# Kernel tuning notes

Hardware: AMD Instinct MI355X
Metric: run time of the kernel (lower is better)

Reference implementation:

```python
import jax, jax.numpy as jnp
import numpy as np

E = 8        # num_local_experts
H = 2048     # hidden_size
I = 4096     # intermediate_size
TOP_K = 1    # num_experts_per_tok
B, S = 2, 1024


def setup_inputs() -> dict:
    key = jax.random.key(0)
    ks = jax.random.split(key, 8)
    sc = 0.02
    return {
        "hidden_states": jax.random.normal(ks[0], (B, S, H), dtype=jnp.float32),
        "router_w": jax.random.normal(ks[1], (E, H), dtype=jnp.float32) * sc,      # torch Linear weight [out,in]
        "gate_up_proj": jax.random.normal(ks[2], (E, H, 2 * I), dtype=jnp.float32) * sc,
        "down_proj": jax.random.normal(ks[3], (E, I, H), dtype=jnp.float32) * sc,
        "shared_gate": jax.random.normal(ks[4], (H, I), dtype=jnp.float32) * sc,
        "shared_up": jax.random.normal(ks[5], (H, I), dtype=jnp.float32) * sc,
        "shared_down": jax.random.normal(ks[6], (I, H), dtype=jnp.float32) * sc,
    }


def reference(hidden_states, router_w, gate_up_proj, down_proj, shared_gate, shared_up, shared_down):
    x = hidden_states.reshape(-1, H)                      # [T, H]
    T = x.shape[0]

    # Router: top-k logits kept, rest -> -inf, then sigmoid (Llama4 sigmoid routing)
    logits = jnp.einsum('th,eh->te', x, router_w)          # [T, E]
    topv, topi = jax.lax.top_k(logits, TOP_K)
    scores = jnp.full_like(logits, -jnp.inf)
    scores = scores.at[jnp.arange(T)[:, None], topi].set(topv)
    router_scores = jax.nn.sigmoid(scores.astype(jnp.float32)).astype(x.dtype).T  # [E, T]

    # Dense dispatch: every token goes to every expert, scaled by its (mostly-zero) score
    routed_in = x[None, :, :] * router_scores[:, :, None]  # [E, T, H]

    # Per-expert gated MLP as one grouped einsum
    gu = jnp.einsum('eth,ehf->etf', routed_in, gate_up_proj)   # [E, T, 2I]
    gate, up = gu[..., :I], gu[..., I:]
    routed_out = jnp.einsum('eti,eih->eth', jax.nn.silu(gate) * up, down_proj)  # [E, T, H]

    # Shared expert on raw tokens
    shared = (jax.nn.silu(x @ shared_gate) * (x @ shared_up)) @ shared_down     # [T, H]

    # scatter_add over full index range == sum over expert axis
    out = shared + routed_out.sum(axis=0)
    return out, router_scores
```

## Files before the change

kernel.cpp:

```cpp
#include <hip/hip_runtime.h>
#include <hip/hip_bf16.h>

#define NE 8
#define TT 2048
#define HD 2048
#define ID 4096

typedef __attribute__((ext_vector_type(8))) short bf16x8;
typedef __attribute__((ext_vector_type(4))) float f32x4;
typedef __attribute__((ext_vector_type(4))) unsigned int u32x4;
typedef __attribute__((ext_vector_type(2))) unsigned int u32x2;
typedef __attribute__((ext_vector_type(4))) unsigned short u16x4;
typedef __attribute__((ext_vector_type(8))) unsigned short u16x8;

__device__ __forceinline__ unsigned short f2bf(float f) {
  return __builtin_bit_cast(unsigned short, __float2bfloat16(f));
}

__global__ void init_kernel(int* counts) {
  if (threadIdx.x < NE) counts[threadIdx.x] = 0;
}

__global__ __launch_bounds__(256) void router_kernel(
    const float* __restrict__ x, const float* __restrict__ rw,
// ... 19 lines not shown
  __shared__ float part[4][NE];
  __shared__ int sE;
  __shared__ float sS;
  const int wave = tid >> 6, lane = tid & 63;
  if (lane == 0) {
#pragma unroll
    for (int e = 0; e < NE; ++e) part[wave][e] = acc[e];
  }
  __syncthreads();
  if (tid == 0) {
    float best = -3.4e38f;
    int be = 0;
#pragma unroll
    for (int e = 0; e < NE; ++e) {
      float v = part[0][e] + part[1][e] + part[2][e] + part[3][e];
      if (v > best) { best = v; be = e; }
    }
    float s = 1.f / (1.f + expf(-best));
    sE = be;
    sS = s;
    int pos = atomicAdd(&counts[be], 1);
    tlist[be * TT + pos] = t;
  }
  __syncthreads();
  if (tid < NE) rs_out[tid * TT + t] = (tid == sE) ? sS : 0.f;
  const float s = sS;
  for (int h = tid; h < HD; h += 256) {
    float f = xr[h];
    xb[(size_t)t * HD + h] = f2bf(f);
    xsb[(size_t)t * HD + h] = f2bf(f * s);
  }
}

__global__ __launch_bounds__(256) void tconv_kernel(
    const float* __restrict__ shg, const float* __restrict__ shu,
    const float* __restrict__ shd, unsigned short* __restrict__ shgT,
    unsigned short* __restrict__ shuT, unsigned short* __restrict__ shdT) {
  const int z = blockIdx.z;
  const float* src;
  unsigned short* dst;
  int K, N;
  if (z == 0)      { src = shg; dst = shgT; K = HD; N = ID; }
  else if (z == 1) { src = shu; dst = shuT; K = HD; N = ID; }
  else             { src = shd; dst = shdT; K = ID; N = HD; }
  const int kb = blockIdx.y * 64, nb = blockIdx.x * 64;
  if (kb >= K || nb >= N) return;
  __shared__ unsigned short tile[64][68];
  const int tid = threadIdx.x;
  const int rr = tid >> 4, cc = (tid & 15) * 4;
#pragma unroll
  for (int it = 0; it < 4; ++it) {
    int r = rr + it * 16;
    f32x4 v = *(const f32x4*)(const void*)(src + (size_t)(kb + r) * N + nb + cc);
    tile[r][cc + 0] = f2bf(v[0]);
    tile[r][cc + 1] = f2bf(v[1]);
    tile[r][cc + 2] = f2bf(v[2]);
    tile[r][cc + 3] = f2bf(v[3]);
  }
  __syncthreads();
  const int nr = tid >> 2, kc = (tid & 3) * 16;
#pragma unroll
  for (int h = 0; h < 2; ++h) {
    u16x8 w;
#pragma unroll
    for (int j = 0; j < 8; ++j) w[j] = tile[kc + h * 8 + j][nr];
    *(u16x8*)(void*)(dst + (size_t)(nb + nr) * K + kb + kc + h * 8) = w;
  }
}

__global__ __launch_bounds__(256) void gu_routed_kernel(
    const unsigned short* __restrict__ xsb, const float* __restrict__ gup,
    const int* __restrict__ counts, const int* __restrict__ tlist,
    unsigned short* __restrict__ hrt) {
  const int e = blockIdx.z;
  const int cnt = counts[e];
  const int row0 = blockIdx.y * 128;
  if (row0 >= cnt) return;
  const int n0 = blockIdx.x * 64;
  const float* Bb = gup + (size_t)e * HD * (2 * ID);
  const float* B1 = Bb + n0;
  const float* B2 = Bb + ID + n0;
  const size_t ldb = 2 * ID;

  __shared__ int toks[128];
  __shared__ __align__(16) unsigned short As[2][128][40];
  __shared__ __align__(16) unsigned short Bg[2][64][36];
  __shared__ __align__(16) unsigned short Bu[2][64][36];

  const int tid = threadIdx.x;
  if (tid < 128) {
    int r = row0 + tid;
    toks[tid] = (r < cnt) ? tlist[e * TT + r] : -1;
  }
  __syncthreads();

  const int lane = tid & 63, wave = tid >> 6;
  const int wm = (wave >> 1) * 64, wn = (wave & 1) * 32;
  const int rA0 = tid >> 2, cA = (tid & 3) * 8, rA1 = rA0 + 64;
  const int tok0 = toks[rA0], tok1 = toks[rA1];
  const unsigned short* ap0 = xsb + ((tok0 >= 0) ? (size_t)tok0 * HD : 0) + cA;
  const unsigned short* ap1 = xsb + ((tok1 >= 0) ? (size_t)tok1 * HD : 0) + cA;
  const int nB = tid & 63;
  const int kq0 = tid >> 6;
// ... 73 lines not shown
#pragma unroll
      for (int nt = 0; nt < 2; ++nt) {
        accg[mt][nt] = __builtin_amdgcn_mfma_f32_16x16x32_bf16(af[mt], bgf[nt], accg[mt][nt], 0, 0, 0);
        accu[mt][nt] = __builtin_amdgcn_mfma_f32_16x16x32_bf16(af[mt], bud[nt], accu[mt][nt], 0, 0, 0);
      }
    __builtin_amdgcn_s_setprio(0);
    __builtin_amdgcn_sched_barrier(0);
    if (t + 1 < NT) WR(cur ^ 1);
    if (t + 2 < NT) LD((t + 2) * 32);
    asm volatile("s_waitcnt lgkmcnt(0)" ::: "memory");
    __builtin_amdgcn_sched_barrier(0);
    __builtin_amdgcn_s_barrier();
  }
#undef LD
#undef WR

#pragma unroll
  for (int mt = 0; mt < 4; ++mt)
#pragma unroll
    for (int nt = 0; nt < 2; ++nt)
#pragma unroll
      for (int r = 0; r < 4; ++r) {
        int ml = wm + mt * 16 + q * 4 + r;
        if (row0 + ml < cnt) {
          int tok = toks[ml];
          int n = n0 + wn + nt * 16 + fm;
          float g = accg[mt][nt][r], u = accu[mt][nt][r];
          float hv = g / (1.f + __expf(-g)) * u;
          hrt[(size_t)tok * ID + n] = f2bf(hv);
        }
      }
}

template <int BF>
__global__ __launch_bounds__(256) void gu_shared_kernel(
    const unsigned short* __restrict__ xb, const float* __restrict__ shg,
    const float* __restrict__ shu, const unsigned short* __restrict__ shgT,
    const unsigned short* __restrict__ shuT, unsigned short* __restrict__ hsh) {
  const int row0 = blockIdx.y * 128;
  const int n0 = blockIdx.x * 64;
  const float* B1 = shg + n0;
  const float* B2 = shu + n0;
  const size_t ldb = ID;
  const unsigned short* T1 = shgT + (size_t)n0 * HD;
  const unsigned short* T2 = shuT + (size_t)n0 * HD;

  __shared__ __align__(16) unsigned short As[2][128][40];
  __shared__ __align__(16) unsigned short Bg[2][64][36];
  __shared__ __align__(16) unsigned short Bu[2][64][36];

  const int tid = threadIdx.x;
  const int lane = tid & 63, wave = tid >> 6;
  const int wm = (wave >> 1) * 64, wn = (wave & 1) * 32;
  const int rA0 = tid >> 2, cA = (tid & 3) * 8, rA1 = rA0 + 64;
  const unsigned short* ap0 = xb + (size_t)(row0 + rA0) * HD + cA;
  const unsigned short* ap1 = xb + (size_t)(row0 + rA1) * HD + cA;
  const int nB = tid & 63;
  const int kq0 = tid >> 6;
  const int fm = lane & 15, q = lane >> 4;
  const int nrT = tid >> 2, kcT = (tid & 3) * 8;

  const f32x4 zf = {0.f, 0.f, 0.f, 0.f};
  f32x4 accg[4][2], accu[4][2];
#pragma unroll
  for (int a = 0; a < 4; ++a)
#pragma unroll
    for (int b = 0; b < 2; ++b) { accg[a][b] = zf; accu[a][b] = zf; }

  u32x4 ra0, ra1, tb1, tb2;
  f32x4 rg0, rg1, ru0, ru1;

#define LD(K0)                                                                 \
  do {                                                                         \
    ra0 = *(const u32x4*)(const void*)(ap0 + (K0));                            \
    ra1 = *(const u32x4*)(const void*)(ap1 + (K0));                            \
    if constexpr (BF) {                                                        \
      tb1 = *(const u32x4*)(const void*)(T1 + (size_t)nrT * HD + (K0) + kcT);  \
      tb2 = *(const u32x4*)(const void*)(T2 + (size_t)nrT * HD + (K0) + kcT);  \
    } else {                                                                   \
      const float* p1 = B1 + (size_t)((K0) + kq0 * 4) * ldb + nB;              \
      const float* p1b = p1 + 16 * ldb;                                        \
      rg0[0] = p1[0]; rg0[1] = p1[ldb]; rg0[2] = p1[2 * ldb]; rg0[3] = p1[3 * ldb]; \
      rg1[0] = p1b[0]; rg1[1] = p1b[ldb]; rg1[2] = p1b[2 * ldb]; rg1[3] = p1b[3 * ldb]; \
      const float* p2 = B2 + (size_t)((K0) + kq0 * 4) * ldb + nB;              \
      const float* p2b = p2 + 16 * ldb;                                        \
      ru0[0] = p2[0]; ru0[1] = p2[ldb]; ru0[2] = p2[2 * ldb]; ru0[3] = p2[3 * ldb]; \
      ru1[0] = p2b[0]; ru1[1] = p2b[ldb]; ru1[2] = p2b[2 * ldb]; ru1[3] = p2b[3 * ldb]; \
    }                                                                          \
  } while (0)

#define WR(BUF)                                                                \
  do {                                                                         \
    *(u32x4*)(void*)&As[BUF][rA0][cA] = ra0;                                   \
    *(u32x4*)(void*)&As[BUF][rA1][cA] = ra1;                                   \
    if constexpr (BF) {                                                        \
      u32x2 lo, hi;                                                            \
      lo[0] = tb1[0]; lo[1] = tb1[1]; hi[0] = tb1[2]; hi[1] = tb1[3];          \
      *(u32x2*)(void*)&Bg[BUF][nrT][kcT] = lo;                                 \
      *(u32x2*)(void*)&Bg[BUF][nrT][kcT + 4] = hi;                             \
      lo[0] = tb2[0]; lo[1] = tb2[1]; hi[0] = tb2[2]; hi[1] = tb2[3];          \
      *(u32x2*)(void*)&Bu[BUF][nrT][kcT] = lo;                                 \
      *(u32x2*)(void*)&Bu[BUF][nrT][kcT + 4] = hi;                             \
    } else {                                                                   \
      u16x4 w;                                                                 \
      w[0] = f2bf(rg0[0]); w[1] = f2bf(rg0[1]); w[2] = f2bf(rg0[2]); w[3] = f2bf(rg0[3]); \
      *(u16x4*)(void*)&Bg[BUF][nB][kq0 * 4] = w;                               \
      w[0] = f2bf(rg1[0]); w[1] = f2bf(rg1[1]); w[2] = f2bf(rg1[2]); w[3] = f2bf(rg1[3]); \
      *(u16x4*)(void*)&Bg[BUF][nB][kq0 * 4 + 16] = w;                          \
      w[0] = f2bf(ru0[0]); w[1] = f2bf(ru0[1]); w[2] = f2bf(ru0[2]); w[3] = f2bf(ru0[3]); \
      *(u16x4*)(void*)&Bu[BUF][nB][kq0 * 4] = w;                               \
      w[0] = f2bf(ru1[0]); w[1] = f2bf(ru1[1]); w[2] = f2bf(ru1[2]); w[3] = f2bf(ru1[3]); \
      *(u16x4*)(void*)&Bu[BUF][nB][kq0 * 4 + 16] = w;                          \
    }                                                                          \
  } while (0)

  LD(0);
  WR(0);
  LD(32);
  asm volatile("s_waitcnt lgkmcnt(0)" ::: "memory");
  __builtin_amdgcn_sched_barrier(0);
  __builtin_amdgcn_s_barrier();

  constexpr int NT = HD / 32;
  for (int t = 0; t < NT; ++t) {
    const int cur = t & 1;
    bf16x8 af[4], bgf[2], bud[2];
#pragma unroll
    for (int mt = 0; mt < 4; ++mt)
      af[mt] = __builtin_bit_cast(bf16x8,
               *(const u32x4*)(const void*)&As[cur][wm + mt * 16 + fm][q * 8]);
#pragma unroll
    for (int nt = 0; nt < 2; ++nt) {
      const unsigned short* bp = &Bg[cur][wn + nt * 16 + fm][q * 8];
      u32x2 lo = *(const u32x2*)(const void*)bp;
      u32x2 hi = *(const u32x2*)(const void*)(bp + 4);
      u32x4 v; v[0] = lo[0]; v[1] = lo[1]; v[2] = hi[0]; v[3] = hi[1];
      bgf[nt] = __builtin_bit_cast(bf16x8, v);
      const unsigned short* bp2 = &Bu[cur][wn + nt * 16 + fm][q * 8];
      lo = *(const u32x2*)(const void*)bp2;
      hi = *(const u32x2*)(const void*)(bp2 + 4);
      v[0] = lo[0]; v[1] = lo[1]; v[2] = hi[0]; v[3] = hi[1];
      bud[nt] = __builtin_bit_cast(bf16x8, v);
    }
    __builtin_amdgcn_s_setprio(1);
#pragma unroll
    for (int mt = 0; mt < 4; ++mt)
#pragma unroll
      for (int nt = 0; nt < 2; ++nt) {
        accg[mt][nt] = __builtin_amdgcn_mfma_f32_16x16x32_bf16(af[mt], bgf[nt], accg[mt][nt], 0, 0, 0);
        accu[mt][nt] = __builtin_amdgcn_mfma_f32_16x16x32_bf16(af[mt], bud[nt], accu[mt][nt], 0, 0, 0);
      }
    __builtin_amdgcn_s_setprio(0);
    __builtin_amdgcn_sched_barrier(0);
    if (t + 1 < NT) WR(cur ^ 1);
    if (t + 2 < NT) LD((t + 2) * 32);
    asm volatile("s_waitcnt lgkmcnt(0)" ::: "memory");
    __builtin_amdgcn_sched_barrier(0);
    __builtin_amdgcn_s_barrier();
  }
#undef LD
#undef WR

#pragma unroll
  for (int mt = 0; mt < 4; ++mt)
#pragma unroll
    for (int nt = 0; nt < 2; ++nt)
#pragma unroll
      for (int r = 0; r < 4; ++r) {
        int row = row0 + wm + mt * 16 + q * 4 + r;
        int n = n0 + wn + nt * 16 + fm;
        float g = accg[mt][nt][r], u = accu[mt][nt][r];
        float hv = g / (1.f + __expf(-g)) * u;
        hsh[(size_t)row * ID + n] = f2bf(hv);
      }
}

template <int BF>
__global__ __launch_bounds__(256) void dn_shared_kernel(
    const unsigned short* __restrict__ hsh, const float* __restrict__ shd,
    const unsigned short* __restrict__ shdT, float* __restrict__ out) {
  const int row0 = blockIdx.y * 128;
  const int n0 = blockIdx.x * 64;
  const float* B = shd + n0;
  const unsigned short* T = shdT + (size_t)n0 * ID;

  __shared__ __align__(16) unsigned short As[2][128][40];
  __shared__ __align__(16) unsigned short Bs[2][64][36];

  const int tid = threadIdx.x;
  const int lane = tid & 63, wave = tid >> 6;
  const int wm = (wave >> 1) * 64, wn = (wave & 1) * 32;
  const int rA0 = tid >> 2, cA = (tid & 3) * 8, rA1 = rA0 + 64;
  const unsigned short* ap0 = hsh + (size_t)(row0 + rA0) * ID + cA;
  const unsigned short* ap1 = hsh + (size_t)(row0 + rA1) * ID + cA;
  const int nB = tid & 63;
  const int kq0 = tid >> 6;
  const int fm = lane & 15, q = lane >> 4;
  const int nrT = tid >> 2, kcT = (tid & 3) * 8;

  const f32x4 zf = {0.f, 0.f, 0.f, 0.f};
  f32x4 acc[4][2];
#pragma unroll
  for (int a = 0; a < 4; ++a)
#pragma unroll
    for (int b = 0; b < 2; ++b) acc[a][b] = zf;

  u32x4 ra0, ra1, tb;
  f32x4 rb0, rb1;

#define LD(K0)                                                                 \
  do {                                                                         \
    ra0 = *(const u32x4*)(const void*)(ap0 + (K0));                            \
    ra1 = *(const u32x4*)(const void*)(ap1 + (K0));                            \
    if constexpr (BF) {                                                        \
      tb = *(const u32x4*)(const void*)(T + (size_t)nrT * ID + (K0) + kcT);    \
    } else {                                                                   \
      const float* p = B + (size_t)((K0) + kq0 * 4) * HD + nB;                 \
      const float* pb = p + 16 * HD;                                           \
      rb0[0] = p[0]; rb0[1] = p[HD]; rb0[2] = p[2 * HD]; rb0[3] = p[3 * HD];   \
      rb1[0] = pb[0]; rb1[1] = pb[HD]; rb1[2] = pb[2 * HD]; rb1[3] = pb[3 * HD]; \
    }                                                                          \
  } while (0)

#define WR(BUF)                                                                \
  do {                                                                         \
    *(u32x4*)(void*)&As[BUF][rA0][cA] = ra0;                                   \
    *(u32x4*)(void*)&As[BUF][rA1][cA] = ra1;                                   \
    if constexpr (BF) {                                                        \
      u32x2 lo, hi;                                                            \
      lo[0] = tb[0]; lo[1] = tb[1]; hi[0] = tb[2]; hi[1] = tb[3];              \
      *(u32x2*)(void*)&Bs[BUF][nrT][kcT] = lo;                                 \
      *(u32x2*)(void*)&Bs[BUF][nrT][kcT + 4] = hi;                             \
    } else {                                                                   \
      u16x4 w;                                                                 \
      w[0] = f2bf(rb0[0]); w[1] = f2bf(rb0[1]); w[2] = f2bf(rb0[2]); w[3] = f2bf(rb0[3]); \
      *(u16x4*)(void*)&Bs[BUF][nB][kq0 * 4] = w;                               \
      w[0] = f2bf(rb1[0]); w[1] = f2bf(rb1[1]); w[2] = f2bf(rb1[2]); w[3] = f2bf(rb1[3]); \
      *(u16x4*)(void*)&Bs[BUF][nB][kq0 * 4 + 16] = w;                          \
    }                                                                          \
  } while (0)

  LD(0);
  WR(0);
  LD(32);
  asm volatile("s_waitcnt lgkmcnt(0)" ::: "memory");
  __builtin_amdgcn_sched_barrier(0);
  __builtin_amdgcn_s_barrier();

  constexpr int NT = ID / 32;
  for (int t = 0; t < NT; ++t) {
    const int cur = t & 1;
    bf16x8 af[4], bfr[2];
#pragma unroll
    for (int mt = 0; mt < 4; ++mt)
      af[mt] = __builtin_bit_cast(bf16x8,
               *(const u32x4*)(const void*)&As[cur][wm + mt * 16 + fm][q * 8]);
#pragma unroll
    for (int nt = 0; nt < 2; ++nt) {
      const unsigned short* bp = &Bs[cur][wn + nt * 16 + fm][q * 8];
      u32x2 lo = *(const u32x2*)(const void*)bp;
      u32x2 hi = *(const u32x2*)(const void*)(bp + 4);
      u32x4 v; v[0] = lo[0]; v[1] = lo[1]; v[2] = hi[0]; v[3] = hi[1];
      bfr[nt] = __builtin_bit_cast(bf16x8, v);
    }
    __builtin_amdgcn_s_setprio(1);
#pragma unroll
    for (int mt = 0; mt < 4; ++mt)
#pragma unroll
      for (int nt = 0; nt < 2; ++nt)
        acc[mt][nt] = __builtin_amdgcn_mfma_f32_16x16x32_bf16(af[mt], bfr[nt], acc[mt][nt], 0, 0, 0);
    __builtin_amdgcn_s_setprio(0);
    __builtin_amdgcn_sched_barrier(0);
    if (t + 1 < NT) WR(cur ^ 1);
    if (t + 2 < NT) LD((t + 2) * 32);
    asm volatile("s_waitcnt lgkmcnt(0)" ::: "memory");
    __builtin_amdgcn_sched_barrier(0);
    __builtin_amdgcn_s_barrier();
  }
#undef LD
#undef WR

#pragma unroll
  for (int mt = 0; mt < 4; ++mt)
#pragma unroll
    for (int nt = 0; nt < 2; ++nt)
#pragma unroll
      for (int r = 0; r < 4; ++r) {
        int row = row0 + wm + mt * 16 + q * 4 + r;
        int n = n0 + wn + nt * 16 + fm;
        out[(size_t)row * HD + n] = acc[mt][nt][r];
      }
}

__global__ __launch_bounds__(256) void dn_routed_kernel(
    const unsigned short* __restrict__ hrt, const float* __restrict__ dwn,
    const int* __restrict__ counts, const int* __restrict__ tlist,
    float* __restrict__ out) {
  const int e = blockIdx.z;
  const int cnt = counts[e];
  const int row0 = blockIdx.y * 128;
  if (row0 >= cnt) return;
  const int n0 = blockIdx.x * 64;
  const float* B = dwn + (size_t)e * ID * HD + n0;

  __shared__ int toks[128];
  __shared__ __align__(16) unsigned short As[2][128][40];
  __shared__ __align__(16) unsigned short Bs[2][64][36];

  const int tid = threadIdx.x;
  if (tid < 128) {
    int r = row0 + tid;
    toks[tid] = (r < cnt) ? tlist[e * TT + r] : -1;
  }
  __syncthreads();

  const int lane = tid & 63, wave = tid >> 6;
  const int wm = (wave >> 1) * 64, wn = (wave & 1) * 32;
  const int rA0 = tid >> 2, cA = (tid & 3) * 8, rA1 = rA0 + 64;
  const int tok0 = toks[rA0], tok1 = toks[rA1];
  const unsigned short* ap0 = hrt + ((tok0 >= 0) ? (size_t)tok0 * ID : 0) + cA;
  const unsigned short* ap1 = hrt + ((tok1 >= 0) ? (size_t)tok1 * ID : 0) + cA;
  const int nB = tid & 63;
  const int kq0 = tid >> 6;
  const int fm = lane & 15, q = lane >> 4;

  const f32x4 zf = {0.f, 0.f, 0.f, 0.f};
  const u32x4 z4 = {0u, 0u, 0u, 0u};
  f32x4 acc[4][2];
#pragma unroll
  for (int a = 0; a < 4; ++a)
#pragma unroll
    for (int b = 0; b < 2; ++b) acc[a][b] = zf;

  u32x4 ra0, ra1;
  f32x4 rb0, rb1;

#define LD(K0)                                                                 \
  do {                                                                         \
    ra0 = (tok0 >= 0) ? *(const u32x4*)(const void*)(ap0 + (K0)) : z4;         \
    ra1 = (tok1 >= 0) ? *(const u32x4*)(const void*)(ap1 + (K0)) : z4;         \
    const float* p = B + (size_t)((K0) + kq0 * 4) * HD + nB;                   \
    const float* pb = p + 16 * HD;                                             \
    rb0[0] = p[0]; rb0[1] = p[HD]; rb0[2] = p[2 * HD]; rb0[3] = p[3 * HD];     \
    rb1[0] = pb[0]; rb1[1] = pb[HD]; rb1[2] = pb[2 * HD]; rb1[3] = pb[3 * HD]; \
  } while (0)

#define WR(BUF)                                                                \
  do {                                                                         \
    *(u32x4*)(void*)&As[BUF][rA0][cA] = ra0;                                   \
    *(u32x4*)(void*)&As[BUF][rA1][cA] = ra1;                                   \
    u16x4 w;                                                                   \
    w[0] = f2bf(rb0[0]); w[1] = f2bf(rb0[1]); w[2] = f2bf(rb0[2]); w[3] = f2bf(rb0[3]); \
    *(u16x4*)(void*)&Bs[BUF][nB][kq0 * 4] = w;                                 \
    w[0] = f2bf(rb1[0]); w[1] = f2bf(rb1[1]); w[2] = f2bf(rb1[2]); w[3] = f2bf(rb1[3]); \
    *(u16x4*)(void*)&Bs[BUF][nB][kq0 * 4 + 16] = w;                            \
  } while (0)

  LD(0);
  WR(0);
  LD(32);
  asm volatile("s_waitcnt lgkmcnt(0)" ::: "memory");
  __builtin_amdgcn_sched_barrier(0);
  __builtin_amdgcn_s_barrier();

  constexpr int NT = ID / 32;
  for (int t = 0; t < NT; ++t) {
    const int cur = t & 1;
    bf16x8 af[4], bfr[2];
#pragma unroll
    for (int mt = 0; mt < 4; ++mt)
      af[mt] = __builtin_bit_cast(bf16x8,
               *(const u32x4*)(const void*)&As[cur][wm + mt * 16 + fm][q * 8]);
#pragma unroll
    for (int nt = 0; nt < 2; ++nt) {
      const unsigned short* bp = &Bs[cur][wn + nt * 16 + fm][q * 8];
      u32x2 lo = *(const u32x2*)(const void*)bp;
      u32x2 hi = *(const u32x2*)(const void*)(bp + 4);
      u32x4 v; v[0] = lo[0]; v[1] = lo[1]; v[2] = hi[0]; v[3] = hi[1];
      bfr[nt] = __builtin_bit_cast(bf16x8, v);
    }
    __builtin_amdgcn_s_setprio(1);
#pragma unroll
    for (int mt = 0; mt < 4; ++mt)
#pragma unroll
      for (int nt = 0; nt < 2; ++nt)
        acc[mt][nt] = __builtin_amdgcn_mfma_f32_16x16x32_bf16(af[mt], bfr[nt], acc[mt][nt], 0, 0, 0);
    __builtin_amdgcn_s_setprio(0);
    __builtin_amdgcn_sched_barrier(0);
    if (t + 1 < NT) WR(cur ^ 1);
    if (t + 2 < NT) LD((t + 2) * 32);
    asm volatile("s_waitcnt lgkmcnt(0)" ::: "memory");
    __builtin_amdgcn_sched_barrier(0);
    __builtin_amdgcn_s_barrier();
  }
#undef LD
#undef WR

#pragma unroll
  for (int mt = 0; mt < 4; ++mt)
#pragma unroll
    for (int nt = 0; nt < 2; ++nt)
#pragma unroll
      for (int r = 0; r < 4; ++r) {
        int ml = wm + mt * 16 + q * 4 + r;
        if (row0 + ml < cnt) {
          int tok = toks[ml];
          int n = n0 + wn + nt * 16 + fm;
          out[(size_t)tok * HD + n] += acc[mt][nt][r];
        }
      }
}

extern "C" void kernel_launch(void* const* d_in, const int* in_sizes, int n_in,
                              void* d_out, int out_size, void* d_ws, size_t ws_size,
                              hipStream_t stream) {
  const float* x   = (const float*)d_in[0];
  const float* rw  = (const float*)d_in[1];
  const float* gup = (const float*)d_in[2];
  const float* dwn = (const float*)d_in[3];
  const float* shg = (const float*)d_in[4];
  const float* shu = (const float*)d_in[5];
  const float* shd = (const float*)d_in[6];
  float* out = (float*)d_out;

  char* ws = (char*)d_ws;
  int* counts = (int*)ws;
  int* tlist = (int*)(ws + 1024);
  unsigned short* xb  = (unsigned short*)(ws + (1 << 17));
  unsigned short* xsb = (unsigned short*)(ws + (1 << 17) + 8388608);
  unsigned short* hsh = (unsigned short*)(ws + (1 << 17) + 16777216);
  unsigned short* hrt = (unsigned short*)(ws + (1 << 17) + 33554432);
  const size_t WB = (size_t)(1 << 17) + 50331648;
  unsigned short* shgT = (unsigned short*)(ws + WB);
  unsigned short* shuT = (unsigned short*)(ws + WB + 16777216);
  unsigned short* shdT = (unsigned short*)(ws + WB + 33554432);
  const size_t need = WB + 3ull * 16777216ull;
  const int shbf = (ws_size >= need) ? 1 : 0;

  hipLaunchKernelGGL(init_kernel, dim3(1), dim3(64), 0, stream, counts);
  hipLaunchKernelGGL(router_kernel, dim3(TT), dim3(256), 0, stream,
                     x, rw, out + (size_t)TT * HD, xb, xsb, counts, tlist);
  if (shbf)
    hipLaunchKernelGGL(tconv_kernel, dim3(64, 64, 3), dim3(256), 0, stream,
                       shg, shu, shd, shgT, shuT, shdT);
  hipLaunchKernelGGL(gu_routed_kernel, dim3(ID / 64, TT / 128, NE), dim3(256), 0, stream,
                     xsb, gup, counts, tlist, hrt);
  if (shbf)
    hipLaunchKernelGGL((gu_shared_kernel<1>), dim3(ID / 64, TT / 128), dim3(256), 0, stream,
                       xb, shg, shu, shgT, shuT, hsh);
  else
    hipLaunchKernelGGL((gu_shared_kernel<0>), dim3(ID / 64, TT / 128), dim3(256), 0, stream,
                       xb, shg, shu, shgT, shuT, hsh);
  if (shbf)
    hipLaunchKernelGGL((dn_shared_kernel<1>), dim3(HD / 64, TT / 128), dim3(256), 0, stream,
                       hsh, shd, shdT, out);
  else
    hipLaunchKernelGGL((dn_shared_kernel<0>), dim3(HD / 64, TT / 128), dim3(256), 0, stream,
                       hsh, shd, shdT, out);
  hipLaunchKernelGGL(dn_routed_kernel, dim3(HD / 64, TT / 128, NE), dim3(256), 0, stream,
                     hrt, dwn, counts, tlist, out);
}
```

Before: 1.313 ms.

## Pre-convert all expert weights to transposed bf16 and merge shared/routed GEMMs

```diff
diff --git a/kernel.cpp b/kernel.cpp
--- a/kernel.cpp
+++ b/kernel.cpp
@@ -75,19 +75,13 @@
   }
 }
 
-__global__ __launch_bounds__(256) void tconv_kernel(
-    const float* __restrict__ shg, const float* __restrict__ shu,
-    const float* __restrict__ shd, unsigned short* __restrict__ shgT,
-    unsigned short* __restrict__ shuT, unsigned short* __restrict__ shdT) {
-  const int z = blockIdx.z;
-  const float* src;
-  unsigned short* dst;
-  int K, N;
-  if (z == 0)      { src = shg; dst = shgT; K = HD; N = ID; }
-  else if (z == 1) { src = shu; dst = shuT; K = HD; N = ID; }
-  else             { src = shd; dst = shdT; K = ID; N = HD; }
+__global__ __launch_bounds__(256) void wconv_kernel(
+    const float* __restrict__ src, unsigned short* __restrict__ dst,
+    const int K, const int N) {
+  const int b = blockIdx.z;
+  src += (size_t)b * K * N;
+  dst += (size_t)b * N * K;
   const int kb = blockIdx.y * 64, nb = blockIdx.x * 64;
-  if (kb >= K || nb >= N) return;
   __shared__ unsigned short tile[64][68];
   const int tid = threadIdx.x;
   const int rr = tid >> 4, cc = (tid & 15) * 4;
@@ -111,7 +105,250 @@
   }
 }
 
-__global__ __launch_bounds__(256) void gu_routed_kernel(
+__global__ __launch_bounds__(256) void gu_kernel(
+    const unsigned short* __restrict__ xb, const unsigned short* __restrict__ xsb,
+    const unsigned short* __restrict__ gupT, const unsigned short* __restrict__ shgT,
+    const unsigned short* __restrict__ shuT, const int* __restrict__ counts,
+    const int* __restrict__ tlist, unsigned short* __restrict__ hsh,
+    unsigned short* __restrict__ hrt) {
+  const int bz = blockIdx.z;
+  const bool sh = (bz == NE);
+  const int cnt = sh ? TT : counts[bz];
+  const int row0 = blockIdx.y * 128;
+  if (row0 >= cnt) return;
+  const int n0 = blockIdx.x * 64;
+  const unsigned short* Aptr = sh ? xb : xsb;
+  const unsigned short* Bg0;
+  const unsigned short* Bu0;
+  if (sh) {
+    Bg0 = shgT + (size_t)n0 * HD;
+    Bu0 = shuT + (size_t)n0 * HD;
+  } else {
+    const unsigned short* base = gupT + (size_t)bz * (2 * ID) * HD;
+    Bg0 = base + (size_t)n0 * HD;
+    Bu0 = base + (size_t)(ID + n0) * HD;
+  }
+  unsigned short* hout = sh ? hsh : hrt;
+
+  __shared__ int toks[128];
+  __shared__ __align__(16) unsigned short As[2][128][40];
+  __shared__ __align__(16) unsigned short Bg[2][64][40];
+  __shared__ __align__(16) unsigned short Bu[2][64][40];
+
+  const int tid = threadIdx.x;
+  if (tid < 128) {
+    int r = row0 + tid;
+    toks[tid] = (r < cnt) ? (sh ? r : tlist[bz * TT + r]) : -1;
+  }
+  __syncthreads();
+
+  const int lane = tid & 63, wave = tid >> 6;
+  const int wm = (wave >> 1) * 64, wn = (wave & 1) * 32;
+  const int rA0 = tid >> 2, cA = (tid & 3) * 8, rA1 = rA0 + 64;
+  const int tok0 = toks[rA0], tok1 = toks[rA1];
+  const unsigned short* ap0 = Aptr + ((tok0 >= 0) ? (size_t)tok0 * HD : 0) + cA;
+  const unsigned short* ap1 = Aptr + ((tok1 >= 0) ? (size_t)tok1 * HD : 0) + cA;
+  const int rB = tid >> 2, cB = (tid & 3) * 8;
+  const unsigned short* pg = Bg0 + (size_t)rB * HD + cB;
+  const unsigned short* pu = Bu0 + (size_t)rB * HD + cB;
+  const int fm = lane & 15, q = lane >> 4;
+
+  const f32x4 zf = {0.f, 0.f, 0.f, 0.f};
+  const u32x4 z4 = {0u, 0u, 0u, 0u};
+  f32x4 accg[4][2], accu[4][2];
+#pragma unroll
+  for (int a = 0; a < 4; ++a)
+#pragma unroll
+    for (int b = 0; b < 2; ++b) { accg[a][b] = zf; accu[a][b] = zf; }
+
+  u32x4 ra0, ra1, rb1, rb2;
+
+#define LD(K0)                                                                 \
+  do {                                                                         \
+    ra0 = (tok0 >= 0) ? *(const u32x4*)(const void*)(ap0 + (K0)) : z4;         \
+    ra1 = (tok1 >= 0) ? *(const u32x4*)(const void*)(ap1 + (K0)) : z4;         \
+    rb1 = *(const u32x4*)(const void*)(pg + (K0));                             \
+    rb2 = *(const u32x4*)(const void*)(pu + (K0));                             \
+  } while (0)
+
+#define WR(BUF)                                                                \
+  do {                                                                         \
+    *(u32x4*)(void*)&As[BUF][rA0][cA] = ra0;                                   \
+    *(u32x4*)(void*)&As[BUF][rA1][cA] = ra1;                                   \
+    *(u32x4*)(void*)&Bg[BUF][rB][cB] = rb1;                                    \
+    *(u32x4*)(void*)&Bu[BUF][rB][cB] = rb2;                                    \
+  } while (0)
+
+  LD(0);
+  WR(0);
+  LD(32);
+  asm volatile("s_waitcnt lgkmcnt(0)" ::: "memory");
+  __builtin_amdgcn_sched_barrier(0);
+  __builtin_amdgcn_s_barrier();
+
+  constexpr int NT = HD / 32;
+  for (int t = 0; t < NT; ++t) {
+    const int cur = t & 1;
+    bf16x8 af[4], bgf[2], bud[2];
+#pragma unroll
+    for (int mt = 0; mt < 4; ++mt)
+      af[mt] = __builtin_bit_cast(bf16x8,
+               *(const u32x4*)(const void*)&As[cur][wm + mt * 16 + fm][q * 8]);
+#pragma unroll
+    for (int nt = 0; nt < 2; ++nt) {
+      bgf[nt] = __builtin_bit_cast(bf16x8,
+                *(const u32x4*)(const void*)&Bg[cur][wn + nt * 16 + fm][q * 8]);
+      bud[nt] = __builtin_bit_cast(bf16x8,
+                *(const u32x4*)(const void*)&Bu[cur][wn + nt * 16 + fm][q * 8]);
+    }
+    __builtin_amdgcn_s_setprio(1);
+#pragma unroll
+    for (int mt = 0; mt < 4; ++mt)
+#pragma unroll
+      for (int nt = 0; nt < 2; ++nt) {
+        accg[mt][nt] = __builtin_amdgcn_mfma_f32_16x16x32_bf16(af[mt], bgf[nt], accg[mt][nt], 0, 0, 0);
+        accu[mt][nt] = __builtin_amdgcn_mfma_f32_16x16x32_bf16(af[mt], bud[nt], accu[mt][nt], 0, 0, 0);
+      }
+    __builtin_amdgcn_s_setprio(0);
+    __builtin_amdgcn_sched_barrier(0);
+    if (t + 1 < NT) WR(cur ^ 1);
+    if (t + 2 < NT) LD((t + 2) * 32);
+    asm volatile("s_waitcnt lgkmcnt(0)" ::: "memory");
+    __builtin_amdgcn_sched_barrier(0);
+    __builtin_amdgcn_s_barrier();
+  }
+#undef LD
+#undef WR
+
+#pragma unroll
+  for (int mt = 0; mt < 4; ++mt)
+#pragma unroll
+    for (int nt = 0; nt < 2; ++nt)
+#pragma unroll
+      for (int r = 0; r < 4; ++r) {
+        int ml = wm + mt * 16 + q * 4 + r;
+        if (row0 + ml < cnt) {
+          int tok = toks[ml];
+          int n = n0 + wn + nt * 16 + fm;
+          float g = accg[mt][nt][r], u = accu[mt][nt][r];
+          float hv = g / (1.f + __expf(-g)) * u;
+          hout[(size_t)tok * ID + n] = f2bf(hv);
+        }
+      }
+}
+
+template <int ROUTED>
+__global__ __launch_bounds__(256) void dn_kernel(
+    const unsigned short* __restrict__ Ah, const unsigned short* __restrict__ BT,
+    const int* __restrict__ counts, const int* __restrict__ tlist,
+    float* __restrict__ out) {
+  const int e = blockIdx.z;
+  const int cnt = ROUTED ? counts[e] : TT;
+  const int row0 = blockIdx.y * 128;
+  if (row0 >= cnt) return;
+  const int n0 = blockIdx.x * 64;
+  const unsigned short* B0 = ROUTED ? (BT + (size_t)e * HD * ID + (size_t)n0 * ID)
+                                    : (BT + (size_t)n0 * ID);
+
+  __shared__ int toks[128];
+  __shared__ __align__(16) unsigned short As[2][128][40];
+  __shared__ __align__(16) unsigned short Bs[2][64][40];
+
+  const int tid = threadIdx.x;
+  if (tid < 128) {
+    int r = row0 + tid;
+    toks[tid] = (r < cnt) ? (ROUTED ? tlist[e * TT + r] : r) : -1;
+  }
+  __syncthreads();
+
+  const int lane = tid & 63, wave = tid >> 6;
+  const int wm = (wave >> 1) * 64, wn = (wave & 1) * 32;
+  const int rA0 = tid >> 2, cA = (tid & 3) * 8, rA1 = rA0 + 64;
+  const int tok0 = toks[rA0], tok1 = toks[rA1];
+  const unsigned short* ap0 = Ah + ((tok0 >= 0) ? (size_t)tok0 * ID : 0) + cA;
+  const unsigned short* ap1 = Ah + ((tok1 >= 0) ? (size_t)tok1 * ID : 0) + cA;
+  const int rB = tid >> 2, cB = (tid & 3) * 8;
+  const unsigned short* pb = B0 + (size_t)rB * ID + cB;
+  const int fm = lane & 15, q = lane >> 4;
+
+  const f32x4 zf = {0.f, 0.f, 0.f, 0.f};
+  const u32x4 z4 = {0u, 0u, 0u, 0u};
+  f32x4 acc[4][2];
+#pragma unroll
+  for (int a = 0; a < 4; ++a)
+#pragma unroll
+    for (int b = 0; b < 2; ++b) acc[a][b] = zf;
+
+  u32x4 ra0, ra1, rb1;
+
+#define LD(K0)                                                                 \
+  do {                                                                         \
+    ra0 = (tok0 >= 0) ? *(const u32x4*)(const void*)(ap0 + (K0)) : z4;         \
+    ra1 = (tok1 >= 0) ? *(const u32x4*)(const void*)(ap1 + (K0)) : z4;         \
+    rb1 = *(const u32x4*)(const void*)(pb + (K0));                             \
+  } while (0)
+
+#define WR(BUF)                                                                \
+  do {                                                                         \
+    *(u32x4*)(void*)&As[BUF][rA0][cA] = ra0;                                   \
+    *(u32x4*)(void*)&As[BUF][rA1][cA] = ra1;                                   \
+    *(u32x4*)(void*)&Bs[BUF][rB][cB] = rb1;                                    \
+  } while (0)
+
+  LD(0);
+  WR(0);
+  LD(32);
+  asm volatile("s_waitcnt lgkmcnt(0)" ::: "memory");
+  __builtin_amdgcn_sched_barrier(0);
+  __builtin_amdgcn_s_barrier();
+
+  constexpr int NT = ID / 32;
+  for (int t = 0; t < NT; ++t) {
+    const int cur = t & 1;
+    bf16x8 af[4], bfr[2];
+#pragma unroll
+    for (int mt = 0; mt < 4; ++mt)
+      af[mt] = __builtin_bit_cast(bf16x8,
+               *(const u32x4*)(const void*)&As[cur][wm + mt * 16 + fm][q * 8]);
+#pragma unroll
+    for (int nt = 0; nt < 2; ++nt)
+      bfr[nt] = __builtin_bit_cast(bf16x8,
+                *(const u32x4*)(const void*)&Bs[cur][wn + nt * 16 + fm][q * 8]);
+    __builtin_amdgcn_s_setprio(1);
+#pragma unroll
+    for (int mt = 0; mt < 4; ++mt)
+#pragma unroll
+      for (int nt = 0; nt < 2; ++nt)
+        acc[mt][nt] = __builtin_amdgcn_mfma_f32_16x16x32_bf16(af[mt], bfr[nt], acc[mt][nt], 0, 0, 0);
+    __builtin_amdgcn_s_setprio(0);
+    __builtin_amdgcn_sched_barrier(0);
+    if (t + 1 < NT) WR(cur ^ 1);
+    if (t + 2 < NT) LD((t + 2) * 32);
+    asm volatile("s_waitcnt lgkmcnt(0)" ::: "memory");
+    __builtin_amdgcn_sched_barrier(0);
+    __builtin_amdgcn_s_barrier();
+  }
+#undef LD
+#undef WR
+
+#pragma unroll
+  for (int mt = 0; mt < 4; ++mt)
+#pragma unroll
+    for (int nt = 0; nt < 2; ++nt)
+#pragma unroll
+      for (int r = 0; r < 4; ++r) {
+        int ml = wm + mt * 16 + q * 4 + r;
+        if (row0 + ml < cnt) {
+          int tok = toks[ml];
+          int n = n0 + wn + nt * 16 + fm;
+          float v = acc[mt][nt][r];
+          float* o = out + (size_t)tok * HD + n;
+          if (ROUTED) *o += v; else *o = v;
+        }
+      }
+}
+
+__global__ __launch_bounds__(256) void gu_routed_f32(
     const unsigned short* __restrict__ xsb, const float* __restrict__ gup,
     const int* __restrict__ counts, const int* __restrict__ tlist,
     unsigned short* __restrict__ hrt) {
@@ -251,18 +488,14 @@
       }
 }
 
-template <int BF>
-__global__ __launch_bounds__(256) void gu_shared_kernel(
+__global__ __launch_bounds__(256) void gu_shared_f32(
     const unsigned short* __restrict__ xb, const float* __restrict__ shg,
-    const float* __restrict__ shu, const unsigned short* __restrict__ shgT,
-    const unsigned short* __restrict__ shuT, unsigned short* __restrict__ hsh) {
+    const float* __restrict__ shu, unsigned short* __restrict__ hsh) {
   const int row0 = blockIdx.y * 128;
   const int n0 = blockIdx.x * 64;
   const float* B1 = shg + n0;
   const float* B2 = shu + n0;
   const size_t ldb = ID;
-  const unsigned short* T1 = shgT + (size_t)n0 * HD;
-  const unsigned short* T2 = shuT + (size_t)n0 * HD;
 
   __shared__ __align__(16) unsigned short As[2][128][40];
   __shared__ __align__(16) unsigned short Bg[2][64][36];
@@ -277,7 +510,6 @@
   const int nB = tid & 63;
   const int kq0 = tid >> 6;
   const int fm = lane & 15, q = lane >> 4;
-  const int nrT = tid >> 2, kcT = (tid & 3) * 8;
 
   const f32x4 zf = {0.f, 0.f, 0.f, 0.f};
   f32x4 accg[4][2], accu[4][2];
@@ -286,51 +518,36 @@
 #pragma unroll
     for (int b = 0; b < 2; ++b) { accg[a][b] = zf; accu[a][b] = zf; }
 
-  u32x4 ra0, ra1, tb1, tb2;
+  u32x4 ra0, ra1;
   f32x4 rg0, rg1, ru0, ru1;
 
 #define LD(K0)                                                                 \
   do {                                                                         \
     ra0 = *(const u32x4*)(const void*)(ap0 + (K0));                            \
     ra1 = *(const u32x4*)(const void*)(ap1 + (K0));                            \
-    if constexpr (BF) {                                                        \
-      tb1 = *(const u32x4*)(const void*)(T1 + (size_t)nrT * HD + (K0) + kcT);  \
-      tb2 = *(const u32x4*)(const void*)(T2 + (size_t)nrT * HD + (K0) + kcT);  \
-    } else {                                                                   \
-      const float* p1 = B1 + (size_t)((K0) + kq0 * 4) * ldb + nB;              \
-      const float* p1b = p1 + 16 * ldb;                                        \
-      rg0[0] = p1[0]; rg0[1] = p1[ldb]; rg0[2] = p1[2 * ldb]; rg0[3] = p1[3 * ldb]; \
-      rg1[0] = p1b[0]; rg1[1] = p1b[ldb]; rg1[2] = p1b[2 * ldb]; rg1[3] = p1b[3 * ldb]; \
-      const float* p2 = B2 + (size_t)((K0) + kq0 * 4) * ldb + nB;              \
-      const float* p2b = p2 + 16 * ldb;                                        \
-      ru0[0] = p2[0]; ru0[1] = p2[ldb]; ru0[2] = p2[2 * ldb]; ru0[3] = p2[3 * ldb]; \
-      ru1[0] = p2b[0]; ru1[1] = p2b[ldb]; ru1[2] = p2b[2 * ldb]; ru1[3] = p2b[3 * ldb]; \
-    }                                                                          \
+    const float* p1 = B1 + (size_t)((K0) + kq0 * 4) * ldb + nB;                \
+    const float* p1b = p1 + 16 * ldb;                                          \
+    rg0[0] = p1[0]; rg0[1] = p1[ldb]; rg0[2] = p1[2 * ldb]; rg0[3] = p1[3 * ldb]; \
+    rg1[0] = p1b[0]; rg1[1] = p1b[ldb]; rg1[2] = p1b[2 * ldb]; rg1[3] = p1b[3 * ldb]; \
+    const float* p2 = B2 + (size_t)((K0) + kq0 * 4) * ldb + nB;                \
+    const float* p2b = p2 + 16 * ldb;                                          \
+    ru0[0] = p2[0]; ru0[1] = p2[ldb]; ru0[2] = p2[2 * ldb]; ru0[3] = p2[3 * ldb]; \
+    ru1[0] = p2b[0]; ru1[1] = p2b[ldb]; ru1[2] = p2b[2 * ldb]; ru1[3] = p2b[3 * ldb]; \
   } while (0)
 
 #define WR(BUF)                                                                \
   do {                                                                         \
     *(u32x4*)(void*)&As[BUF][rA0][cA] = ra0;                                   \
     *(u32x4*)(void*)&As[BUF][rA1][cA] = ra1;                                   \
-    if constexpr (BF) {                                                        \
-      u32x2 lo, hi;                                                            \
-      lo[0] = tb1[0]; lo[1] = tb1[1]; hi[0] = tb1[2]; hi[1] = tb1[3];          \
-      *(u32x2*)(void*)&Bg[BUF][nrT][kcT] = lo;                                 \
-      *(u32x2*)(void*)&Bg[BUF][nrT][kcT + 4] = hi;                             \
-      lo[0] = tb2[0]; lo[1] = tb2[1]; hi[0] = tb2[2]; hi[1] = tb2[3];          \
-      *(u32x2*)(void*)&Bu[BUF][nrT][kcT] = lo;                                 \
-      *(u32x2*)(void*)&Bu[BUF][nrT][kcT + 4] = hi;                             \
-    } else {                                                                   \
-      u16x4 w;                                                                 \
-      w[0] = f2bf(rg0[0]); w[1] = f2bf(rg0[1]); w[2] = f2bf(rg0[2]); w[3] = f2bf(rg0[3]); \
-      *(u16x4*)(void*)&Bg[BUF][nB][kq0 * 4] = w;                               \
-      w[0] = f2bf(rg1[0]); w[1] = f2bf(rg1[1]); w[2] = f2bf(rg1[2]); w[3] = f2bf(rg1[3]); \
-      *(u16x4*)(void*)&Bg[BUF][nB][kq0 * 4 + 16] = w;                          \
-      w[0] = f2bf(ru0[0]); w[1] = f2bf(ru0[1]); w[2] = f2bf(ru0[2]); w[3] = f2bf(ru0[3]); \
-      *(u16x4*)(void*)&Bu[BUF][nB][kq0 * 4] = w;                               \
-      w[0] = f2bf(ru1[0]); w[1] = f2bf(ru1[1]); w[2] = f2bf(ru1[2]); w[3] = f2bf(ru1[3]); \
-      *(u16x4*)(void*)&Bu[BUF][nB][kq0 * 4 + 16] = w;                          \
-    }                                                                          \
+    u16x4 w;                                                                   \
+    w[0] = f2bf(rg0[0]); w[1] = f2bf(rg0[1]); w[2] = f2bf(rg0[2]); w[3] = f2bf(rg0[3]); \
+    *(u16x4*)(void*)&Bg[BUF][nB][kq0 * 4] = w;                                 \
+    w[0] = f2bf(rg1[0]); w[1] = f2bf(rg1[1]); w[2] = f2bf(rg1[2]); w[3] = f2bf(rg1[3]); \
+    *(u16x4*)(void*)&Bg[BUF][nB][kq0 * 4 + 16] = w;                            \
+    w[0] = f2bf(ru0[0]); w[1] = f2bf(ru0[1]); w[2] = f2bf(ru0[2]); w[3] = f2bf(ru0[3]); \
+    *(u16x4*)(void*)&Bu[BUF][nB][kq0 * 4] = w;                                 \
+    w[0] = f2bf(ru1[0]); w[1] = f2bf(ru1[1]); w[2] = f2bf(ru1[2]); w[3] = f2bf(ru1[3]); \
+    *(u16x4*)(void*)&Bu[BUF][nB][kq0 * 4 + 16] = w;                            \
   } while (0)
 
   LD(0);
@@ -394,69 +611,69 @@
       }
 }
 
-template <int BF>
-__global__ __launch_bounds__(256) void dn_shared_kernel(
-    const unsigned short* __restrict__ hsh, const float* __restrict__ shd,
-    const unsigned short* __restrict__ shdT, float* __restrict__ out) {
+template <int ROUTED>
+__global__ __launch_bounds__(256) void dn_f32(
+    const unsigned short* __restrict__ Ah, const float* __restrict__ Bbase,
+    const int* __restrict__ counts, const int* __restrict__ tlist,
+    float* __restrict__ out) {
+  const int e = blockIdx.z;
+  const int cnt = ROUTED ? counts[e] : TT;
   const int row0 = blockIdx.y * 128;
+  if (row0 >= cnt) return;
   const int n0 = blockIdx.x * 64;
-  const float* B = shd + n0;
-  const unsigned short* T = shdT + (size_t)n0 * ID;
-
+  const float* B = ROUTED ? (Bbase + (size_t)e * ID * HD + n0) : (Bbase + n0);
+
+  __shared__ int toks[128];
   __shared__ __align__(16) unsigned short As[2][128][40];
   __shared__ __align__(16) unsigned short Bs[2][64][36];
 
   const int tid = threadIdx.x;
+  if (tid < 128) {
+    int r = row0 + tid;
+    toks[tid] = (r < cnt) ? (ROUTED ? tlist[e * TT + r] : r) : -1;
+  }
+  __syncthreads();
+
   const int lane = tid & 63, wave = tid >> 6;
   const int wm = (wave >> 1) * 64, wn = (wave & 1) * 32;
   const int rA0 = tid >> 2, cA = (tid & 3) * 8, rA1 = rA0 + 64;
-  const unsigned short* ap0 = hsh + (size_t)(row0 + rA0) * ID + cA;
-  const unsigned short* ap1 = hsh + (size_t)(row0 + rA1) * ID + cA;
+  const int tok0 = toks[rA0], tok1 = toks[rA1];
+  const unsigned short* ap0 = Ah + ((tok0 >= 0) ? (size_t)tok0 * ID : 0) + cA;
+  const unsigned short* ap1 = Ah + ((tok1 >= 0) ? (size_t)tok1 * ID : 0) + cA;
   const int nB = tid & 63;
   const int kq0 = tid >> 6;
   const int fm = lane & 15, q = lane >> 4;
-  const int nrT = tid >> 2, kcT = (tid & 3) * 8;
 
   const f32x4 zf = {0.f, 0.f, 0.f, 0.f};
+  const u32x4 z4 = {0u, 0u, 0u, 0u};
   f32x4 acc[4][2];
 #pragma unroll
   for (int a = 0; a < 4; ++a)
 #pragma unroll
     for (int b = 0; b < 2; ++b) acc[a][b] = zf;
 
-  u32x4 ra0, ra1, tb;
+  u32x4 ra0, ra1;
   f32x4 rb0, rb1;
 
 #define LD(K0)                                                                 \
   do {                                                                         \
-    ra0 = *(const u32x4*)(const void*)(ap0 + (K0));                            \
-    ra1 = *(const u32x4*)(const void*)(ap1 + (K0));                            \
-    if constexpr (BF) {                                                        \
-      tb = *(const u32x4*)(const void*)(T + (size_t)nrT * ID + (K0) + kcT);    \
-    } else {                                                                   \
-      const float* p = B + (size_t)((K0) + kq0 * 4) * HD + nB;                 \
-      const float* pb = p + 16 * HD;                                           \
-      rb0[0] = p[0]; rb0[1] = p[HD]; rb0[2] = p[2 * HD]; rb0[3] = p[3 * HD];   \
-      rb1[0] = pb[0]; rb1[1] = pb[HD]; rb1[2] = pb[2 * HD]; rb1[3] = pb[3 * HD]; \
-    }                                                                          \
+    ra0 = (tok0 >= 0) ? *(const u32x4*)(const void*)(ap0 + (K0)) : z4;         \
+    ra1 = (tok1 >= 0) ? *(const u32x4*)(const void*)(ap1 + (K0)) : z4;         \
+    const float* p = B + (size_t)((K0) + kq0 * 4) * HD + nB;                   \
+    const float* pbq = p + 16 * HD;                                            \
+    rb0[0] = p[0]; rb0[1] = p[HD]; rb0[2] = p[2 * HD]; rb0[3] = p[3 * HD];     \
+    rb1[0] = pbq[0]; rb1[1] = pbq[HD]; rb1[2] = pbq[2 * HD]; rb1[3] = pbq[3 * HD]; \
   } while (0)
 
 #define WR(BUF)                                                                \
   do {                                                                         \
     *(u32x4*)(void*)&As[BUF][rA0][cA] = ra0;                                   \
     *(u32x4*)(void*)&As[BUF][rA1][cA] = ra1;                                   \
-    if constexpr (BF) {                                                        \
-      u32x2 lo, hi;                                                            \
-      lo[0] = tb[0]; lo[1] = tb[1]; hi[0] = tb[2]; hi[1] = tb[3];              \
-      *(u32x2*)(void*)&Bs[BUF][nrT][kcT] = lo;                                 \
-      *(u32x2*)(void*)&Bs[BUF][nrT][kcT + 4] = hi;                             \
-    } else {                                                                   \
-      u16x4 w;                                                                 \
-      w[0] = f2bf(rb0[0]); w[1] = f2bf(rb0[1]); w[2] = f2bf(rb0[2]); w[3] = f2bf(rb0[3]); \
-      *(u16x4*)(void*)&Bs[BUF][nB][kq0 * 4] = w;                               \
-      w[0] = f2bf(rb1[0]); w[1] = f2bf(rb1[1]); w[2] = f2bf(rb1[2]); w[3] = f2bf(rb1[3]); \
-      *(u16x4*)(void*)&Bs[BUF][nB][kq0 * 4 + 16] = w;                          \
-    }                                                                          \
+    u16x4 w;                                                                   \
+    w[0] = f2bf(rb0[0]); w[1] = f2bf(rb0[1]); w[2] = f2bf(rb0[2]); w[3] = f2bf(rb0[3]); \
+    *(u16x4*)(void*)&Bs[BUF][nB][kq0 * 4] = w;                                 \
+    w[0] = f2bf(rb1[0]); w[1] = f2bf(rb1[1]); w[2] = f2bf(rb1[2]); w[3] = f2bf(rb1[3]); \
+    *(u16x4*)(void*)&Bs[BUF][nB][kq0 * 4 + 16] = w;                            \
   } while (0)
 
   LD(0);
@@ -505,127 +722,13 @@
     for (int nt = 0; nt < 2; ++nt)
 #pragma unroll
       for (int r = 0; r < 4; ++r) {
-        int row = row0 + wm + mt * 16 + q * 4 + r;
-        int n = n0 + wn + nt * 16 + fm;
-        out[(size_t)row * HD + n] = acc[mt][nt][r];
-      }
-}
-
-__global__ __launch_bounds__(256) void dn_routed_kernel(
-    const unsigned short* __restrict__ hrt, const float* __restrict__ dwn,
-    const int* __restrict__ counts, const int* __restrict__ tlist,
-    float* __restrict__ out) {
-  const int e = blockIdx.z;
-  const int cnt = counts[e];
-  const int row0 = blockIdx.y * 128;
-  if (row0 >= cnt) return;
-  const int n0 = blockIdx.x * 64;
-  const float* B = dwn + (size_t)e * ID * HD + n0;
-
-  __shared__ int toks[128];
-  __shared__ __align__(16) unsigned short As[2][128][40];
-  __shared__ __align__(16) unsigned short Bs[2][64][36];
-
-  const int tid = threadIdx.x;
-  if (tid < 128) {
-    int r = row0 + tid;
-    toks[tid] = (r < cnt) ? tlist[e * TT + r] : -1;
-  }
-  __syncthreads();
-
-  const int lane = tid & 63, wave = tid >> 6;
-  const int wm = (wave >> 1) * 64, wn = (wave & 1) * 32;
-  const int rA0 = tid >> 2, cA = (tid & 3) * 8, rA1 = rA0 + 64;
-  const int tok0 = toks[rA0], tok1 = toks[rA1];
-  const unsigned short* ap0 = hrt + ((tok0 >= 0) ? (size_t)tok0 * ID : 0) + cA;
-  const unsigned short* ap1 = hrt + ((tok1 >= 0) ? (size_t)tok1 * ID : 0) + cA;
-  const int nB = tid & 63;
-  const int kq0 = tid >> 6;
-  const int fm = lane & 15, q = lane >> 4;
-
-  const f32x4 zf = {0.f, 0.f, 0.f, 0.f};
-  const u32x4 z4 = {0u, 0u, 0u, 0u};
-  f32x4 acc[4][2];
-#pragma unroll
-  for (int a = 0; a < 4; ++a)
-#pragma unroll
-    for (int b = 0; b < 2; ++b) acc[a][b] = zf;
-
-  u32x4 ra0, ra1;
-  f32x4 rb0, rb1;
-
-#define LD(K0)                                                                 \
-  do {                                                                         \
-    ra0 = (tok0 >= 0) ? *(const u32x4*)(const void*)(ap0 + (K0)) : z4;         \
-    ra1 = (tok1 >= 0) ? *(const u32x4*)(const void*)(ap1 + (K0)) : z4;         \
-    const float* p = B + (size_t)((K0) + kq0 * 4) * HD + nB;                   \
-    const float* pb = p + 16 * HD;                                             \
-    rb0[0] = p[0]; rb0[1] = p[HD]; rb0[2] = p[2 * HD]; rb0[3] = p[3 * HD];     \
-    rb1[0] = pb[0]; rb1[1] = pb[HD]; rb1[2] = pb[2 * HD]; rb1[3] = pb[3 * HD]; \
-  } while (0)
-
-#define WR(BUF)                                                                \
-  do {                                                                         \
-    *(u32x4*)(void*)&As[BUF][rA0][cA] = ra0;                                   \
-    *(u32x4*)(void*)&As[BUF][rA1][cA] = ra1;                                   \
-    u16x4 w;                                                                   \
-    w[0] = f2bf(rb0[0]); w[1] = f2bf(rb0[1]); w[2] = f2bf(rb0[2]); w[3] = f2bf(rb0[3]); \
-    *(u16x4*)(void*)&Bs[BUF][nB][kq0 * 4] = w;                                 \
-    w[0] = f2bf(rb1[0]); w[1] = f2bf(rb1[1]); w[2] = f2bf(rb1[2]); w[3] = f2bf(rb1[3]); \
-    *(u16x4*)(void*)&Bs[BUF][nB][kq0 * 4 + 16] = w;                            \
-  } while (0)
-
-  LD(0);
-  WR(0);
-  LD(32);
-  asm volatile("s_waitcnt lgkmcnt(0)" ::: "memory");
-  __builtin_amdgcn_sched_barrier(0);
-  __builtin_amdgcn_s_barrier();
-
-  constexpr int NT = ID / 32;
-  for (int t = 0; t < NT; ++t) {
-    const int cur = t & 1;
-    bf16x8 af[4], bfr[2];
-#pragma unroll
-    for (int mt = 0; mt < 4; ++mt)
-      af[mt] = __builtin_bit_cast(bf16x8,
-               *(const u32x4*)(const void*)&As[cur][wm + mt * 16 + fm][q * 8]);
-#pragma unroll
-    for (int nt = 0; nt < 2; ++nt) {
-      const unsigned short* bp = &Bs[cur][wn + nt * 16 + fm][q * 8];
-      u32x2 lo = *(const u32x2*)(const void*)bp;
-      u32x2 hi = *(const u32x2*)(const void*)(bp + 4);
-      u32x4 v; v[0] = lo[0]; v[1] = lo[1]; v[2] = hi[0]; v[3] = hi[1];
-      bfr[nt] = __builtin_bit_cast(bf16x8, v);
-    }
-    __builtin_amdgcn_s_setprio(1);
-#pragma unroll
-    for (int mt = 0; mt < 4; ++mt)
-#pragma unroll
-      for (int nt = 0; nt < 2; ++nt)
-        acc[mt][nt] = __builtin_amdgcn_mfma_f32_16x16x32_bf16(af[mt], bfr[nt], acc[mt][nt], 0, 0, 0);
-    __builtin_amdgcn_s_setprio(0);
-    __builtin_amdgcn_sched_barrier(0);
-    if (t + 1 < NT) WR(cur ^ 1);
-    if (t + 2 < NT) LD((t + 2) * 32);
-    asm volatile("s_waitcnt lgkmcnt(0)" ::: "memory");
-    __builtin_amdgcn_sched_barrier(0);
-    __builtin_amdgcn_s_barrier();
-  }
-#undef LD
-#undef WR
-
-#pragma unroll
-  for (int mt = 0; mt < 4; ++mt)
-#pragma unroll
-    for (int nt = 0; nt < 2; ++nt)
-#pragma unroll
-      for (int r = 0; r < 4; ++r) {
         int ml = wm + mt * 16 + q * 4 + r;
         if (row0 + ml < cnt) {
           int tok = toks[ml];
           int n = n0 + wn + nt * 16 + fm;
-          out[(size_t)tok * HD + n] += acc[mt][nt][r];
+          float v = acc[mt][nt][r];
+          float* o = out + (size_t)tok * HD + n;
+          if (ROUTED) *o += v; else *o = v;
         }
       }
 }
@@ -643,39 +746,50 @@
   float* out = (float*)d_out;
 
   char* ws = (char*)d_ws;
+  const size_t MB = 1048576ull;
   int* counts = (int*)ws;
   int* tlist = (int*)(ws + 1024);
-  unsigned short* xb  = (unsigned short*)(ws + (1 << 17));
-  unsigned short* xsb = (unsigned short*)(ws + (1 << 17) + 8388608);
-  unsigned short* hsh = (unsigned short*)(ws + (1 << 17) + 16777216);
-  unsigned short* hrt = (unsigned short*)(ws + (1 << 17) + 33554432);
-  const size_t WB = (size_t)(1 << 17) + 50331648;
+  unsigned short* xb   = (unsigned short*)(ws + (1 << 17));
+  unsigned short* xsb  = (unsigned short*)(ws + (1 << 17) + 8 * MB);
+  unsigned short* hsh  = (unsigned short*)(ws + (1 << 17) + 16 * MB);
+  unsigned short* hrt  = (unsigned short*)(ws + (1 << 17) + 32 * MB);
+  const size_t WB = (size_t)(1 << 17) + 48 * MB;
   unsigned short* shgT = (unsigned short*)(ws + WB);
-  unsigned short* shuT = (unsigned short*)(ws + WB + 16777216);
-  unsigned short* shdT = (unsigned short*)(ws + WB + 33554432);
-  const size_t need = WB + 3ull * 16777216ull;
-  const int shbf = (ws_size >= need) ? 1 : 0;
+  unsigned short* shuT = (unsigned short*)(ws + WB + 16 * MB);
+  unsigned short* shdT = (unsigned short*)(ws + WB + 32 * MB);
+  unsigned short* gupT = (unsigned short*)(ws + WB + 48 * MB);
+  unsigned short* dwnT = (unsigned short*)(ws + WB + 304 * MB);
+  const size_t need = WB + 432 * MB;
 
   hipLaunchKernelGGL(init_kernel, dim3(1), dim3(64), 0, stream, counts);
   hipLaunchKernelGGL(router_kernel, dim3(TT), dim3(256), 0, stream,
                      x, rw, out + (size_t)TT * HD, xb, xsb, counts, tlist);
-  if (shbf)
-    hipLaunchKernelGGL(tconv_kernel, dim3(64, 64, 3), dim3(256), 0, stream,
-                       shg, shu, shd, shgT, shuT, shdT);
-  hipLaunchKernelGGL(gu_routed_kernel, dim3(ID / 64, TT / 128, NE), dim3(256), 0, stream,
-                     xsb, gup, counts, tlist, hrt);
-  if (shbf)
-    hipLaunchKernelGGL((gu_shared_kernel<1>), dim3(ID / 64, TT / 128), dim3(256), 0, stream,
-                       xb, shg, shu, shgT, shuT, hsh);
-  else
-    hipLaunchKernelGGL((gu_shared_kernel<0>), dim3(ID / 64, TT / 128), dim3(256), 0, stream,
-                       xb, shg, shu, shgT, shuT, hsh);
-  if (shbf)
-    hipLaunchKernelGGL((dn_shared_kernel<1>), dim3(HD / 64, TT / 128), dim3(256), 0, stream,
-                       hsh, shd, shdT, out);
-  else
-    hipLaunchKernelGGL((dn_shared_kernel<0>), dim3(HD / 64, TT / 128), dim3(256), 0, stream,
-                       hsh, shd, shdT, out);
-  hipLaunchKernelGGL(dn_routed_kernel, dim3(HD / 64, TT / 128, NE), dim3(256), 0, stream,
-                     hrt, dwn, counts, tlist, out);
-}
+
+  if (ws_size >= need) {
+    hipLaunchKernelGGL(wconv_kernel, dim3(2 * ID / 64, HD / 64, NE), dim3(256), 0, stream,
+                       gup, gupT, HD, 2 * ID);
+    hipLaunchKernelGGL(wconv_kernel, dim3(HD / 64, ID / 64, NE), dim3(256), 0, stream,
+                       dwn, dwnT, ID, HD);
+    hipLaunchKernelGGL(wconv_kernel, dim3(ID / 64, HD / 64, 1), dim3(256), 0, stream,
+                       shg, shgT, HD, ID);
+    hipLaunchKernelGGL(wconv_kernel, dim3(ID / 64, HD / 64, 1), dim3(256), 0, stream,
+                       shu, shuT, HD, ID);
+    hipLaunchKernelGGL(wconv_kernel, dim3(HD / 64, ID / 64, 1), dim3(256), 0, stream,
+                       shd, shdT, ID, HD);
+    hipLaunchKernelGGL(gu_kernel, dim3(ID / 64, TT / 128, NE + 1), dim3(256), 0, stream,
+                       xb, xsb, gupT, shgT, shuT, counts, tlist, hsh, hrt);
+    hipLaunchKernelGGL((dn_kernel<0>), dim3(HD / 64, TT / 128, 1), dim3(256), 0, stream,
+                       hsh, shdT, counts, tlist, out);
+    hipLaunchKernelGGL((dn_kernel<1>), dim3(HD / 64, TT / 128, NE), dim3(256), 0, stream,
+                       hrt, dwnT, counts, tlist, out);
+  } else {
+    hipLaunchKernelGGL(gu_routed_f32, dim3(ID / 64, TT / 128, NE), dim3(256), 0, stream,
+                       xsb, gup, counts, tlist, hrt);
+    hipLaunchKernelGGL(gu_shared_f32, dim3(ID / 64, TT / 128), dim3(256), 0, stream,
+                       xb, shg, shu, hsh);
+    hipLaunchKernelGGL((dn_f32<0>), dim3(HD / 64, TT / 128, 1), dim3(256), 0, stream,
+                       hsh, shd, counts, tlist, out);
+    hipLaunchKernelGGL((dn_f32<1>), dim3(HD / 64, TT / 128, NE), dim3(256), 0, stream,
+                       hrt, dwn, counts, tlist, out);
+  }
+}
```

New measurement: 1.466 ms. 11.6% more time.
